# Kernel optimization log

Hardware: AMD Instinct MI355X
Metric: run time of the kernel (lower is better)

The kernel has to match this reference:

```python
import jax, jax.numpy as jnp
import numpy as np

B, T, HM = 2, 2048, 1024
HEADS = 16
DK = (HM // 2) // HEADS   # expand_k = 0.5 -> key_dim 512, per-head 32
DV = HM // HEADS          # expand_v = 1.0 -> per-head 64
LOW_RANK = 16             # gate low-rank dim (fla default)
GATE_NORM = 16.0          # gate_logit_normalizer (fla default)
EPS = 1e-5


def setup_inputs() -> dict:
    key = jax.random.key(0)
    ks = jax.random.split(key, 12)
    def p(k, shape, s=0.02):
        return jax.random.normal(k, shape, jnp.float32) * s
    return dict(
        x=jax.random.normal(ks[0], (B, T, HM), jnp.float32),
        ln_w=jnp.ones((HM,), jnp.float32), ln_b=jnp.zeros((HM,), jnp.float32),
        Wq=p(ks[1], (HM, HEADS * DK)), Wk=p(ks[2], (HM, HEADS * DK)),
        Wv=p(ks[3], (HM, HEADS * DV)),
        gk_w1=p(ks[4], (HM, LOW_RANK)), gk_w2=p(ks[5], (LOW_RANK, HEADS * DK)),
        gk_b2=jnp.zeros((HEADS * DK,), jnp.float32),
        Wg=p(ks[6], (HM, HEADS * DV)), rms_w=jnp.ones((DV,), jnp.float32),
        Wo=p(ks[7], (HEADS * DV, HM)),
        W1=p(ks[8], (HM, 2 * HM)), b1=jnp.zeros((2 * HM,), jnp.float32),
        W2=p(ks[9], (2 * HM, HM)), b2=jnp.zeros((HM,), jnp.float32),
    )


def _ln(x, w, b):
    m = x.mean(-1, keepdims=True)
    v = ((x - m) ** 2).mean(-1, keepdims=True)
    return (x - m) * jax.lax.rsqrt(v + EPS) * w + b


def _rms(x, w):
    return x * jax.lax.rsqrt((x * x).mean(-1, keepdims=True) + EPS) * w


def _gla(q, k, v, gk):
    # gated linear attention recurrence:
    # S_t = diag(exp(gk_t)) S_{t-1} + k_t v_t^T ;  o_t = q_t S_t
    # q,k,gk: [B,T,H,DK], v: [B,T,H,DV]
    def step(S, inp):
        qt, kt, vt, gt = inp
        S = jnp.exp(gt)[..., None] * S + kt[..., None] * vt[..., None, :]
        return S, jnp.einsum('bhk,bhkv->bhv', qt, S)
    xs = tuple(jnp.moveaxis(a, 1, 0) for a in (q, k, v, gk))
    S0 = jnp.zeros((q.shape[0], q.shape[2], q.shape[3], v.shape[3]), q.dtype)
    _, o = jax.lax.scan(step, S0, xs)
    return jnp.moveaxis(o, 0, 1)


def reference(x, ln_w, ln_b, Wq, Wk, Wv, gk_w1, gk_w2, gk_b2, Wg, rms_w, Wo, W1, b1, W2, b2):
    Bb, Tt, _ = x.shape
    h = _ln(x, ln_w, ln_b)
    q = (h @ Wq).reshape(Bb, Tt, HEADS, DK)
    k = (h @ Wk).reshape(Bb, Tt, HEADS, DK)
    v = (h @ Wv).reshape(Bb, Tt, HEADS, DV)
    gk = (jax.nn.log_sigmoid((h @ gk_w1) @ gk_w2 + gk_b2) / GATE_NORM)
    gk = gk.reshape(Bb, Tt, HEADS, DK)
    o = _gla(q * (DK ** -0.5), k, v, gk)
    # output gate: RMSNorm(o) * swish(g)  (FusedRMSNormSwishGate)
    g = (h @ Wg).reshape(Bb, Tt, HEADS, DV)
    o = _rms(o, rms_w) * (g * jax.nn.sigmoid(g))
    x = x + o.reshape(Bb, Tt, HEADS * DV) @ Wo
    h2 = _ln(x, ln_w, ln_b)  # same shared norm module
    return x + jax.nn.gelu(h2 @ W1 + b1, approximate=False) @ W2 + b2
```

## Files before the change

### kernel.cpp

```cpp
#include <hip/hip_runtime.h>
#include <hip/hip_bf16.h>
#include <math.h>


using bf16 = __hip_bfloat16;
typedef __attribute__((ext_vector_type(8))) short bf16x8;
typedef __attribute__((ext_vector_type(4))) float f32x4;

#define BT 4096
#define HM 1024
#define DK 32
#define DV 64
#define NC 32
#define CHK 64

#if defined(__has_builtin)
#if __has_builtin(__builtin_amdgcn_global_load_lds)
#define HAVE_GLDS 1
#endif
#endif

#ifdef HAVE_GLDS
#define GLDS16(g, l) __builtin_amdgcn_global_load_lds( \
    (const __attribute__((address_space(1))) unsigned int*)(g), \
    (__attribute__((address_space(3))) unsigned int*)(l), 16, 0, 0)
#else
#define GLDS16(g, l) (*(int4*)(l) = *(const int4*)(g))
#endif

__device__ __forceinline__ float b2f(bf16 v) { return __bfloat162float(v); }
__device__ __forceinline__ bf16 f2b(float v) { return __float2bfloat16(v); }
__device__ __forceinline__ float clampf(float v, float lim) {
    return fminf(fmaxf(v, -lim), lim);
}
__device__ __forceinline__ float lo16(unsigned int u) {
    union { unsigned int i; float f; } c; c.i = u << 16; return c.f;
}
__device__ __forceinline__ float hi16(unsigned int u) {
    union { unsigned int i; float f; } c; c.i = u & 0xffff0000u; return c.f;
}
__device__ __forceinline__ void acc8(float a, uint4 r, float* o) {
    o[0] += a * lo16(r.x); o[1] += a * hi16(r.x);
    o[2] += a * lo16(r.y); o[3] += a * hi16(r.y);
    o[4] += a * lo16(r.z); o[5] += a * hi16(r.z);
    o[6] += a * lo16(r.w); o[7] += a * hi16(r.w);
}

__global__ __launch_bounds__(256) void detect_dtype(
    const unsigned int* __restrict__ x, int* __restrict__ flag)
{
    int tid = threadIdx.x;
    int cnt = 0;
    for (int i = 0; i < 16; ++i) {
        unsigned int w = x[tid * 16 + i];
        unsigned int e_lo = (w >> 7) & 0xffu;
        unsigned int e_hi = (w >> 23) & 0xffu;
        cnt += (e_lo >= 110 && e_lo <= 135 && e_hi >= 110 && e_hi <= 135) ? 1 : 0;
    }
    __shared__ int red[256];
    red[tid] = cnt;
    __syncthreads();
    for (int s = 128; s > 0; s >>= 1) {
        if (tid < s) red[tid] += red[tid + s];
        __syncthreads();
    }
    if (tid == 0) *flag = (red[0] > 2048) ? 1 : 0;
}

struct SmallCvt { const void* s[8]; bf16* d[8]; int n[8]; };
__global__ __launch_bounds__(256) void cvt_small(SmallCvt sc, const int* __restrict__ flag)
{
    bool isb = (*flag != 0);
    int stride = gridDim.x * 256;
    #pragma unroll
    for (int seg = 0; seg < 8; ++seg) {
        int n = sc.n[seg];
        for (int i = blockIdx.x * 256 + threadIdx.x; i < n; i += stride) {
            if (isb) ((ushort*)sc.d[seg])[i] = ((const ushort*)sc.s[seg])[i];
            else     sc.d[seg][i] = f2b(((const float*)sc.s[seg])[i]);
        }
    }
}

struct TDesc { const void* src; ushort* dst; int R, C, tile0; };
struct TAll { TDesc d[7]; };
__global__ __launch_bounds__(256) void transpose_all(
    TAll ta, const int* __restrict__ flag)
{
    bool isb = (*flag != 0);
    int bid = blockIdx.x;
    int seg = 0;
    #pragma unroll
    for (int i = 1; i < 7; ++i) if (bid >= ta.d[i].tile0) seg = i;
    const void* src = ta.d[seg].src;
    ushort* dst = ta.d[seg].dst;
    int R = ta.d[seg].R, C = ta.d[seg].C;
    int t = bid - ta.d[seg].tile0;
    int tilesX = C >> 5;
    int c0 = (t % tilesX) * 32, r0 = (t / tilesX) * 32;

    __shared__ ushort tile[32][33];
    int x = threadIdx.x, y = threadIdx.y;
    #pragma unroll
    for (int dy = 0; dy < 32; dy += 8) {
        size_t idx = (size_t)(r0 + y + dy) * C + c0 + x;
        ushort v;
        if (isb) v = ((const ushort*)src)[idx];
        else { bf16 tb = f2b(((const float*)src)[idx]); v = *(ushort*)&tb; }
        tile[y + dy][x] = v;
    }
    __syncthreads();
    #pragma unroll
    for (int dy = 0; dy < 32; dy += 8)
        dst[(size_t)(c0 + y + dy) * R + r0 + x] = tile[x][y + dy];
}

template <int DO_GK>
__global__ __launch_bounds__(256) void ln_kernel(
    const void* __restrict__ x, const bf16* __restrict__ w, const bf16* __restrict__ b,
    bf16* __restrict__ out, const int* __restrict__ flag, int force,
    const bf16* __restrict__ w1, const bf16* __restrict__ w2,
    const bf16* __restrict__ b2i, bf16* __restrict__ gkout)
{
    bool isb = (force >= 0) ? (force != 0) : (*flag != 0);
    size_t base = (size_t)blockIdx.x * HM;
    int tid = threadIdx.x;
    float v[4], s = 0.f, s2 = 0.f;
    #pragma unroll
    for (int u = 0; u < 4; ++u) {
        size_t idx = base + tid + u * 256;
        float f = isb ? b2f(((const bf16*)x)[idx]) : ((const float*)x)[idx];
        v[u] = f; s += f; s2 += f * f;
    }
    #pragma unroll
    for (int off = 32; off >= 1; off >>= 1) {
        s  += __shfl_down(s, off);
        s2 += __shfl_down(s2, off);
    }
    __shared__ float ra[4], rb[4];
    __shared__ float hrow[1024];
    int wave = tid >> 6;
    if ((tid & 63) == 0) { ra[wave] = s; rb[wave] = s2; }
    __syncthreads();
    s = ra[0] + ra[1] + ra[2] + ra[3];
    s2 = rb[0] + rb[1] + rb[2] + rb[3];
    float mean = s * (1.f / HM);
    float var = fmaxf(s2 * (1.f / HM) - mean * mean, 0.f);
    float rs = rsqrtf(var + 1e-5f);
    #pragma unroll
    for (int u = 0; u < 4; ++u) {
        int col = tid + u * 256;
        float h = (v[u] - mean) * rs * b2f(w[col]) + b2f(b[col]);
        out[base + col] = f2b(h);
        if constexpr (DO_GK) hrow[col] = h;
    }
    if constexpr (DO_GK) {
        __syncthreads();
        int d = tid & 15, seg = tid >> 4;
        float sg = 0.f;
        #pragma unroll 8
        for (int j = 0; j < 64; ++j) {
            int i = seg * 64 + j;
            sg += hrow[i] * b2f(w1[i * 16 + d]);
        }
        __shared__ float red[256];
        __shared__ float g1[16];
        red[tid] = sg;
        __syncthreads();
        if (tid < 16) {
            float t = 0.f;
            #pragma unroll
            for (int s2i = 0; s2i < 16; ++s2i) t += red[s2i * 16 + tid];
            g1[tid] = t;
        }
        __syncthreads();
        #pragma unroll
        for (int rep = 0; rep < 2; ++rep) {
            int n = tid + rep * 256;
            float z = b2f(b2i[n]);
            #pragma unroll
            for (int r = 0; r < 16; ++r) z += g1[r] * b2f(w2[r * 512 + n]);
            z = clampf(z, 30.f);
            float ls = (z >= 0.f) ? -log1pf(expf(-z)) : (z - log1pf(expf(z)));
            gkout[blockIdx.x * 512 + n] = f2b(ls * 0.0625f);
        }
    }
}

template <int BN, int MODE>
__global__ __launch_bounds__(512, 2) void gemm8p(
    const bf16* __restrict__ A, const bf16* __restrict__ Wt,
    const bf16* __restrict__ bias, const void* __restrict__ resid,
    void* __restrict__ out, int M, int N, int K, const int* __restrict__ oflag)
{
    constexpr int NFRAG  = BN / 128;
    constexpr int BLOADS = (BN == 256) ? 2 : 1;

    extern __shared__ ushort sm[];
    ushort* smA = sm;
    ushort* smB = sm + 32768;

    int tid = threadIdx.x;
    int wid = tid >> 6, l = tid & 63;
    int wm = wid >> 2, wn = wid & 3;
    int r16 = l & 15, quad = l >> 4;
    int bm = blockIdx.x * 256, bn = blockIdx.y * BN;
    bool isb = false;
    if constexpr (MODE == 1 || MODE == 3) isb = (*oflag != 0);

    const ushort* Au = (const ushort*)A;
    const ushort* Wu = (const ushort*)Wt;
    const int NT = K >> 6;

    auto stageA = [&](int t, int h) {
        #pragma unroll
        for (int i = 0; i < 2; ++i) {
            int j = i * 512 + tid;
            int lr = j >> 3, slot = j & 7;
            int r = (lr & 63) + h * 64 + (lr >> 6) * 128;
            int sl = slot ^ (r & 7);
            const ushort* g = Au + (size_t)(bm + r) * K + t * 64 + sl * 8;
            GLDS16(g, &smA[(t & 1) * 16384 + r * 64 + slot * 8]);
        }
    };
    auto stageB = [&](int t, int h) {
        #pragma unroll
        for (int i = 0; i < BLOADS; ++i) {
            int j = i * 512 + tid;
            int lr = j >> 3, slot = j & 7;
            int r = (BN == 256) ? ((lr & 31) + h * 32 + (lr >> 5) * 64)
                                : ((lr & 15) + h * 16 + (lr >> 4) * 32);
            int sl = slot ^ (r & 7);
            const ushort* g = Wu + (size_t)(bn + r) * K + t * 64 + sl * 8;
            GLDS16(g, &smB[(t & 1) * (BN * 64) + r * 64 + slot * 8]);
        }
    };

    int colx0 = (quad * 8) ^ ((r16 & 7) * 8);
    int colx1 = colx0 ^ 32;

    f32x4 acc[8][BN / 64] = {};

    stageA(0, 0); stageB(0, 0); stageA(0, 1); stageB(0, 1);
    if (NT > 1) { stageA(1, 0); stageB(1, 1); }
    if constexpr (BN == 256) asm volatile("s_waitcnt vmcnt(4)" ::: "memory");
    else                     asm volatile("s_waitcnt vmcnt(3)" ::: "memory");
    __builtin_amdgcn_s_barrier();

    for (int t = 0; t < NT; ++t) {
        const int abase = (t & 1) * 16384;
        const int bbase = (t & 1) * (BN * 64);
        #pragma unroll
        for (int q = 0; q < 4; ++q) {
            const int mh = q >> 1;
            const int nh = (q == 1 || q == 2) ? 1 : 0;
            bf16x8 af[2][4], bw[2][NFRAG];
            #pragma unroll
            for (int mf = 0; mf < 4; ++mf) {
                int r = wm * 128 + mh * 64 + mf * 16 + r16;
                af[0][mf] = *(const bf16x8*)&smA[abase + r * 64 + colx0];
                af[1][mf] = *(const bf16x8*)&smA[abase + r * 64 + colx1];
            }
            #pragma unroll
            for (int nf = 0; nf < NFRAG; ++nf) {
                int r = wn * (BN / 4) + nh * (NFRAG * 16) + nf * 16 + r16;
                bw[0][nf] = *(const bf16x8*)&smB[bbase + r * 64 + colx0];
                bw[1][nf] = *(const bf16x8*)&smB[bbase + r * 64 + colx1];
            }
            if (q == 0) { if (t + 1 < NT) stageA(t + 1, 1); }
            if (q == 1) { if (t + 1 < NT) stageB(t + 1, 0); }
            if (q == 2) { if (t + 2 < NT) stageA(t + 2, 0); }
            if (q == 3) { if (t + 2 < NT) stageB(t + 2, 1); }
            __builtin_amdgcn_s_barrier();
            asm volatile("s_waitcnt lgkmcnt(0)" ::: "memory");
            __builtin_amdgcn_s_setprio(1);
            #pragma unroll
            for (int mf = 0; mf < 4; ++mf)
                #pragma unroll
                for (int nf = 0; nf < NFRAG; ++nf) {
                    f32x4& a = acc[mh * 4 + mf][nh * NFRAG + nf];
                    a = __builtin_amdgcn_mfma_f32_16x16x32_bf16(af[0][mf], bw[0][nf], a, 0, 0, 0);
                    a = __builtin_amdgcn_mfma_f32_16x16x32_bf16(af[1][mf], bw[1][nf], a, 0, 0, 0);
                }
            __builtin_amdgcn_s_setprio(0);
            if (q == 3) {
                if (t + 2 < NT) {
                    if constexpr (BN == 256) asm volatile("s_waitcnt vmcnt(4)" ::: "memory");
                    else                     asm volatile("s_waitcnt vmcnt(3)" ::: "memory");
                } else {
                    asm volatile("s_waitcnt vmcnt(0)" ::: "memory");
                }
            }
            __builtin_amdgcn_s_barrier();
        }
    }

    #pragma unroll
    for (int am = 0; am < 8; ++am) {
        int row0 = bm + wm * 128 + am * 16 + quad * 4;
        #pragma unroll
        for (int an = 0; an < BN / 64; ++an) {
            int col = bn + wn * (BN / 4) + an * 16 + r16;
            #pragma unroll
            for (int r = 0; r < 4; ++r) {
                size_t idx = (size_t)(row0 + r) * N + col;
                float v = acc[am][an][r];
                if constexpr (MODE == 0) {
                    ((bf16*)out)[idx] = f2b(clampf(v, 1e4f));
                } else if constexpr (MODE == 2) {
                    float t = clampf(v + b2f(bias[col]), 50.f);
                    ((bf16*)out)[idx] = f2b(0.5f * t * (1.f + erff(t * 0.70710678f)));
                } else if constexpr (MODE == 1) {
                    float rv = isb ? b2f(((const bf16*)resid)[idx])
                                   : ((const float*)resid)[idx];
                    ((float*)out)[idx] = clampf(rv + v, 1e5f);
                } else {
                    float t = clampf(v + b2f(bias[col]) + ((const float*)resid)[idx], 2e5f);
                    if (isb) ((bf16*)out)[idx] = f2b(t);
                    else     ((float*)out)[idx] = t;
                }
            }
        }
    }
}

__global__ __launch_bounds__(256) void gla_phase1(
    const bf16* __restrict__ gkb, const bf16* __restrict__ qvg,
    float* __restrict__ clbuf, float* __restrict__ Dbuf, float* __restrict__ Pbuf)
{
    int bh = blockIdx.x, c = blockIdx.y;
    int b = bh >> 4, hh = bh & 15;
    int row0 = b * 2048 + c * CHK;
    __shared__ float glog[CHK][DK + 1];
    __shared__ float wk[CHK][DK + 1];
    __shared__ float segsum[8][DK + 1];
    __shared__ __align__(16) ushort vt[CHK][DV];
    int tid = threadIdx.x;
    int k = tid & 31, i8 = (tid >> 5) * 8;
    int seg = tid >> 5;
    #pragma unroll
    for (int u = 0; u < 8; ++u) {
        int i = i8 + u;
        float g = b2f(gkb[(size_t)(row0 + i) * 512 + hh * 32 + k]);
        glog[i][k] = fminf(fmaxf(g, -2.f), 0.f);
    }
    {
        int cc = tid & 7, ii = tid >> 3;
        #pragma unroll
        for (int h = 0; h < 2; ++h) {
            int i = ii + h * 32;
            uint4 val = *(const uint4*)((const ushort*)qvg + (size_t)(row0 + i) * 3072 + 1024 + hh * 64 + cc * 8);
            *(uint4*)&vt[i][cc * 8] = val;
        }
    }
    __syncthreads();
    {
        float run = 0.f;
        #pragma unroll
        for (int u = 0; u < 8; ++u) {
            run += glog[i8 + u][k];
            glog[i8 + u][k] = run;
        }
        segsum[seg][k] = run;
    }
    __syncthreads();
    {
        float off = 0.f;
        for (int s = 0; s < seg; ++s) off += segsum[s][k];
        #pragma unroll
        for (int u = 0; u < 8; ++u) glog[i8 + u][k] += off;
    }
    __syncthreads();
    #pragma unroll
    for (int u = 0; u < 8; ++u) {
        int i = i8 + u;
        float cl = glog[i][k];
        float cl63 = glog[CHK - 1][k];
        clbuf[(size_t)(row0 + i) * 512 + hh * 32 + k] = cl;
        wk[i][k] = expf(fmaxf(cl63 - cl, -60.f)) *
            b2f(qvg[(size_t)(row0 + i) * 3072 + 512 + hh * 32 + k]);
    }
    if (tid < 32) Dbuf[(size_t)(bh * 32 + c) * 32 + tid] = expf(glog[CHK - 1][tid]);
    __syncthreads();
    int kk = tid >> 3, v8 = (tid & 7) * 8;
    float acc[8] = {};
    for (int j = 0; j < CHK; ++j) {
        float w = wk[j][kk];
        uint4 raw = *(const uint4*)&vt[j][v8];
        acc8(w, raw, acc);
    }
    float* Pp = Pbuf + (size_t)(bh * 32 + c) * 2048 + kk * 64 + v8;
    #pragma unroll
    for (int u = 0; u < 8; ++u) Pp[u] = acc[u];
}

__global__ __launch_bounds__(256) void gla_scan(
    const float* __restrict__ Pbuf, const float* __restrict__ Dbuf,
    float* __restrict__ Sbuf)
{
    int bh = blockIdx.x >> 3, vg8 = blockIdx.x & 7;
    int kk = threadIdx.x >> 3, vv = vg8 * 8 + (threadIdx.x & 7);
    float S = 0.f;
    for (int c = 0; c < NC; ++c) {
        size_t idx = (size_t)(bh * 32 + c) * 2048 + kk * 64 + vv;
        float P = Pbuf[idx];
        float D = Dbuf[(size_t)(bh * 32 + c) * 32 + kk];
        Sbuf[idx] = S;
        S = D * S + P;
    }
}

__global__ __launch_bounds__(256) void gla_phase3(
    const bf16* __restrict__ qvg,
    const float* __restrict__ clbuf, const float* __restrict__ Sbuf,
    const bf16* __restrict__ rmsw, bf16* __restrict__ obuf)
{
    int bh = blockIdx.x, c = blockIdx.y;
    int b = bh >> 4, hh = bh & 15;
    int row0 = b * 2048 + c * CHK;
    __shared__ float qs[CHK][36], ks[CHK][36];
    __shared__ float S0[DK][68];
    __shared__ float Amat[CHK][CHK + 1];
    __shared__ __align__(16) ushort vt[CHK][DV];
    int tid = threadIdx.x;
    {
        int k = tid & 31, i8 = (tid >> 5) * 8;
        #pragma unroll
        for (int u = 0; u < 8; ++u) {
            int i = i8 + u;
            size_t r = (size_t)(row0 + i);
            int col = hh * 32 + k;
            float cl = fmaxf(clbuf[r * 512 + col], -60.f);
            qs[i][k] = b2f(qvg[r * 3072 + col]) * expf(cl) * 0.17677669529663687f;
            ks[i][k] = b2f(qvg[r * 3072 + 512 + col]) * expf(-cl);
        }
    }
    {
        int cc = tid & 7, ii = tid >> 3;
        #pragma unroll
        for (int h = 0; h < 2; ++h) {
            int i = ii + h * 32;
            uint4 val = *(const uint4*)((const ushort*)qvg + (size_t)(row0 + i) * 3072 + 1024 + hh * 64 + cc * 8);
            *(uint4*)&vt[i][cc * 8] = val;
        }
    }
    {
        int kk = tid >> 3, v8 = (tid & 7) * 8;
        const float* Sp = Sbuf + (size_t)(bh * 32 + c) * 2048 + kk * 64 + v8;
        *(f32x4*)&S0[kk][v8]     = *(const f32x4*)Sp;
        *(f32x4*)&S0[kk][v8 + 4] = *(const f32x4*)(Sp + 4);
    }
    __syncthreads();
    int i = tid >> 2, jb = tid & 3;
    for (int jj = 0; jj < 16; ++jj) {
        int j = jb + jj * 4;
        float d = 0.f;
        if (j <= i) {
            const f32x4* qp = (const f32x4*)qs[i];
            const f32x4* kp = (const f32x4*)ks[j];
            #pragma unroll
            for (int q8 = 0; q8 < 8; ++q8) {
                f32x4 a = qp[q8], bq = kp[q8];
                d += a.x * bq.x + a.y * bq.y + a.z * bq.z + a.w * bq.w;
            }
        }
        Amat[i][j] = d;
    }
    __syncthreads();
    float o[16] = {};
    int vv = jb * 16;
    for (int j = 0; j < CHK; ++j) {
        float a = Amat[i][j];
        uint4 r0 = *(const uint4*)&vt[j][vv];
        uint4 r1 = *(const uint4*)&vt[j][vv + 8];
        acc8(a, r0, o);
        acc8(a, r1, o + 8);
    }
    #pragma unroll
    for (int kk = 0; kk < DK; ++kk) {
        float qv = qs[i][kk];
        const f32x4* Sp = (const f32x4*)&S0[kk][vv];
        #pragma unroll
        for (int q4 = 0; q4 < 4; ++q4) {
            f32x4 sv = Sp[q4];
            o[q4 * 4 + 0] += qv * sv.x; o[q4 * 4 + 1] += qv * sv.y;
            o[q4 * 4 + 2] += qv * sv.z; o[q4 * 4 + 3] += qv * sv.w;
        }
    }
    float ss = 0.f;
    #pragma unroll
    for (int u = 0; u < 16; ++u) ss += o[u] * o[u];
    ss += __shfl_xor(ss, 1);
    ss += __shfl_xor(ss, 2);
    float sc = rsqrtf(fmaxf(ss, 0.f) * (1.f / DV) + 1e-5f);
    size_t r = (size_t)(row0 + i);
    #pragma unroll
    for (int u = 0; u < 16; ++u) {
        float g = b2f(qvg[r * 3072 + 2048 + hh * 64 + vv + u]);
        float sw = g / (1.f + expf(-g));
        obuf[r * 1024 + hh * 64 + vv + u] = f2b(clampf(o[u] * sc * b2f(rmsw[vv + u]) * sw, 3e4f));
    }
}

extern "C" void kernel_launch(void* const* d_in, const int* in_sizes, int n_in,
                              void* d_out, int out_size, void* d_ws, size_t ws_size,
                              hipStream_t stream) {
    (void)in_sizes; (void)n_in; (void)out_size; (void)ws_size;

    char* ws = (char*)d_ws;
    const size_t MB = 1024 * 1024;
    const size_t KB = 1024;
    bf16*  WqkT = (bf16*)(ws + 0);
    bf16*  WkT  = (bf16*)(ws + 1 * MB);
    bf16*  WvgT = (bf16*)(ws + 2 * MB);
    bf16*  WgT  = (bf16*)(ws + 4 * MB);
    bf16*  WoT  = (bf16*)(ws + 6 * MB);
    bf16*  W1T  = (bf16*)(ws + 8 * MB);
    bf16*  W2T  = (bf16*)(ws + 12 * MB);
    bf16*  hbuf = (bf16*)(ws + 16 * MB);
    bf16*  qvg  = (bf16*)(ws + 24 * MB);
    bf16*  gkb  = (bf16*)(ws + 48 * MB);
    float* clbf = (float*)(ws + 52 * MB);
    float* Dbuf = (float*)(ws + 60 * MB);
    float* Pbuf = (float*)(ws + 61 * MB);
    float* Sbuf = (float*)(ws + 69 * MB);
    bf16*  obuf = (bf16*)(ws + 61 * MB);
    float* ybuf = (float*)(ws + 32 * MB);
    bf16*  f1   = (bf16*)(ws + 48 * MB);
    bf16*  clnw = (bf16*)(ws + 85 * MB);
    bf16*  clnb = (bf16*)(ws + 85 * MB + 64 * KB);
    bf16*  cgw1 = (bf16*)(ws + 85 * MB + 128 * KB);
    bf16*  cgw2 = (bf16*)(ws + 85 * MB + 192 * KB);
    bf16*  cgb2 = (bf16*)(ws + 85 * MB + 256 * KB);
    bf16*  crms = (bf16*)(ws + 85 * MB + 320 * KB);
    bf16*  cb1  = (bf16*)(ws + 85 * MB + 384 * KB);
    bf16*  cb2  = (bf16*)(ws + 85 * MB + 448 * KB);
    int*   flag = (int*)(ws + 85 * MB + 512 * KB);

    hipLaunchKernelGGL(detect_dtype, dim3(1), dim3(256), 0, stream,
                       (const unsigned int*)d_in[0], flag);

    SmallCvt sc;
    sc.s[0] = d_in[1];  sc.d[0] = clnw; sc.n[0] = 1024;
    sc.s[1] = d_in[2];  sc.d[1] = clnb; sc.n[1] = 1024;
    sc.s[2] = d_in[6];  sc.d[2] = cgw1; sc.n[2] = 16384;
    sc.s[3] = d_in[7];  sc.d[3] = cgw2; sc.n[3] = 8192;
    sc.s[4] = d_in[8];  sc.d[4] = cgb2; sc.n[4] = 512;
    sc.s[5] = d_in[10]; sc.d[5] = crms; sc.n[5] = 64;
    sc.s[6] = d_in[13]; sc.d[6] = cb1;  sc.n[6] = 2048;
    sc.s[7] = d_in[15]; sc.d[7] = cb2;  sc.n[7] = 1024;
    hipLaunchKernelGGL(cvt_small, dim3(64), dim3(256), 0, stream, sc, flag);

    TAll ta;
    ta.d[0] = { d_in[3],  (ushort*)WqkT, 1024, 512,  0 };
    ta.d[1] = { d_in[4],  (ushort*)WkT,  1024, 512,  512 };
    ta.d[2] = { d_in[5],  (ushort*)WvgT, 1024, 1024, 1024 };
    ta.d[3] = { d_in[9],  (ushort*)WgT,  1024, 1024, 2048 };
    ta.d[4] = { d_in[11], (ushort*)WoT,  1024, 1024, 3072 };
    ta.d[5] = { d_in[12], (ushort*)W1T,  1024, 2048, 4096 };
    ta.d[6] = { d_in[14], (ushort*)W2T,  2048, 1024, 6144 };
    hipLaunchKernelGGL(transpose_all, dim3(8192), dim3(32, 8), 0, stream, ta, flag);

    hipLaunchKernelGGL((ln_kernel<1>), dim3(BT), dim3(256), 0, stream,
                       d_in[0], clnw, clnb, hbuf, (const int*)flag, -1,
                       cgw1, cgw2, cgb2, gkb);

    hipLaunchKernelGGL((gemm8p<256, 0>), dim3(16, 12), dim3(512), 131072, stream,
                       hbuf, WqkT, (const bf16*)nullptr, nullptr, (void*)qvg,
                       BT, 3072, 1024, flag);

    hipLaunchKernelGGL(gla_phase1, dim3(32, 32), dim3(256), 0, stream, gkb, qvg, clbf, Dbuf, Pbuf);
    hipLaunchKernelGGL(gla_scan, dim3(256), dim3(256), 0, stream, Pbuf, Dbuf, Sbuf);
    hipLaunchKernelGGL(gla_phase3, dim3(32, 32), dim3(256), 0, stream, qvg, clbf, Sbuf, crms, obuf);

    hipLaunchKernelGGL((gemm8p<128, 1>), dim3(16, 8), dim3(512), 98304, stream,
                       obuf, WoT, (const bf16*)nullptr, (const void*)d_in[0], (void*)ybuf,
                       BT, 1024, 1024, flag);
    hipLaunchKernelGGL((ln_kernel<0>), dim3(BT), dim3(256), 0, stream,
                       (const void*)ybuf, clnw, clnb, hbuf, (const int*)flag, 0,
                       (const bf16*)nullptr, (const bf16*)nullptr, (const bf16*)nullptr, (bf16*)nullptr);
    hipLaunchKernelGGL((gemm8p<128, 2>), dim3(16, 16), dim3(512), 98304, stream,
                       hbuf, W1T, cb1, nullptr, (void*)f1, BT, 2048, 1024, flag);
    hipLaunchKernelGGL((gemm8p<128, 3>), dim3(16, 8), dim3(512), 98304, stream,
                       f1, W2T, cb2, (const void*)ybuf, d_out, BT, 1024, 2048, flag);
}
```

Before: 396.6 us.

## Restructure GEMM inner loop into K-halves with reused B fragments and static LDS

The GEMM main loop now splits each 64-wide K tile into two 32-wide halves across the four sub-steps. All N fragments of B are loaded once per half and reused across both M halves, instead of loading A and B for both K halves at every sub-step. The staging order of A and B loads and the vmcnt waits are reordered to match, and shared memory moves from dynamic to static arrays. This lowers LDS read traffic per MFMA but holds more B registers live, which may affect occupancy or stall behaviour.

After: 397.8 us. No clear change (+0.3%).

```diff
diff --git a/kernel.cpp b/kernel.cpp
--- a/kernel.cpp
+++ b/kernel.cpp
@@ -193,12 +193,11 @@
     const bf16* __restrict__ bias, const void* __restrict__ resid,
     void* __restrict__ out, int M, int N, int K, const int* __restrict__ oflag)
 {
-    constexpr int NFRAG  = BN / 128;
-    constexpr int BLOADS = (BN == 256) ? 2 : 1;
-
-    extern __shared__ ushort sm[];
-    ushort* smA = sm;
-    ushort* smB = sm + 32768;
+    constexpr int NF = BN / 64;
+    constexpr int BLOADS = BN / 128;
+
+    __shared__ __align__(16) ushort smA[2 * 256 * 64];
+    __shared__ __align__(16) ushort smB[2 * BN * 64];
 
     int tid = threadIdx.x;
     int wid = tid >> 6, l = tid & 63;
@@ -236,40 +235,41 @@
         }
     };
 
-    int colx0 = (quad * 8) ^ ((r16 & 7) * 8);
-    int colx1 = colx0 ^ 32;
-
-    f32x4 acc[8][BN / 64] = {};
-
-    stageA(0, 0); stageB(0, 0); stageA(0, 1); stageB(0, 1);
-    if (NT > 1) { stageA(1, 0); stageB(1, 1); }
+    const int colx0 = (quad ^ (r16 & 7)) * 8;
+
+    f32x4 acc[8][NF] = {};
+
+    stageA(0, 0); stageA(0, 1); stageB(0, 0); stageB(0, 1);
+    if (NT > 1) { stageB(1, 0); stageB(1, 1); }
     if constexpr (BN == 256) asm volatile("s_waitcnt vmcnt(4)" ::: "memory");
-    else                     asm volatile("s_waitcnt vmcnt(3)" ::: "memory");
+    else                     asm volatile("s_waitcnt vmcnt(2)" ::: "memory");
     __builtin_amdgcn_s_barrier();
 
     for (int t = 0; t < NT; ++t) {
         const int abase = (t & 1) * 16384;
         const int bbase = (t & 1) * (BN * 64);
+        bf16x8 bw[2][NF];
         #pragma unroll
         for (int q = 0; q < 4; ++q) {
             const int mh = q >> 1;
-            const int nh = (q == 1 || q == 2) ? 1 : 0;
-            bf16x8 af[2][4], bw[2][NFRAG];
+            const int kh = q & 1;
+            const int colx = kh ? (colx0 ^ 32) : colx0;
+            bf16x8 af[4];
             #pragma unroll
             for (int mf = 0; mf < 4; ++mf) {
                 int r = wm * 128 + mh * 64 + mf * 16 + r16;
-                af[0][mf] = *(const bf16x8*)&smA[abase + r * 64 + colx0];
-                af[1][mf] = *(const bf16x8*)&smA[abase + r * 64 + colx1];
+                af[mf] = *(const bf16x8*)&smA[abase + r * 64 + colx];
             }
-            #pragma unroll
-            for (int nf = 0; nf < NFRAG; ++nf) {
-                int r = wn * (BN / 4) + nh * (NFRAG * 16) + nf * 16 + r16;
-                bw[0][nf] = *(const bf16x8*)&smB[bbase + r * 64 + colx0];
-                bw[1][nf] = *(const bf16x8*)&smB[bbase + r * 64 + colx1];
+            if (q < 2) {
+                #pragma unroll
+                for (int nf = 0; nf < NF; ++nf) {
+                    int r = wn * (BN / 4) + nf * 16 + r16;
+                    bw[kh][nf] = *(const bf16x8*)&smB[bbase + r * 64 + colx];
+                }
             }
-            if (q == 0) { if (t + 1 < NT) stageA(t + 1, 1); }
-            if (q == 1) { if (t + 1 < NT) stageB(t + 1, 0); }
-            if (q == 2) { if (t + 2 < NT) stageA(t + 2, 0); }
+            if (q == 0) { if (t + 1 < NT) stageA(t + 1, 0); }
+            if (q == 1) { if (t + 1 < NT) stageA(t + 1, 1); }
+            if (q == 2) { if (t + 2 < NT) stageB(t + 2, 0); }
             if (q == 3) { if (t + 2 < NT) stageB(t + 2, 1); }
             __builtin_amdgcn_s_barrier();
             asm volatile("s_waitcnt lgkmcnt(0)" ::: "memory");
@@ -277,16 +277,14 @@
             #pragma unroll
             for (int mf = 0; mf < 4; ++mf)
                 #pragma unroll
-                for (int nf = 0; nf < NFRAG; ++nf) {
-                    f32x4& a = acc[mh * 4 + mf][nh * NFRAG + nf];
-                    a = __builtin_amdgcn_mfma_f32_16x16x32_bf16(af[0][mf], bw[0][nf], a, 0, 0, 0);
-                    a = __builtin_amdgcn_mfma_f32_16x16x32_bf16(af[1][mf], bw[1][nf], a, 0, 0, 0);
-                }
+                for (int nf = 0; nf < NF; ++nf)
+                    acc[mh * 4 + mf][nf] = __builtin_amdgcn_mfma_f32_16x16x32_bf16(
+                        af[mf], bw[kh][nf], acc[mh * 4 + mf][nf], 0, 0, 0);
             __builtin_amdgcn_s_setprio(0);
             if (q == 3) {
                 if (t + 2 < NT) {
                     if constexpr (BN == 256) asm volatile("s_waitcnt vmcnt(4)" ::: "memory");
-                    else                     asm volatile("s_waitcnt vmcnt(3)" ::: "memory");
+                    else                     asm volatile("s_waitcnt vmcnt(2)" ::: "memory");
                 } else {
                     asm volatile("s_waitcnt vmcnt(0)" ::: "memory");
                 }
@@ -299,7 +297,7 @@
     for (int am = 0; am < 8; ++am) {
         int row0 = bm + wm * 128 + am * 16 + quad * 4;
         #pragma unroll
-        for (int an = 0; an < BN / 64; ++an) {
+        for (int an = 0; an < NF; ++an) {
             int col = bn + wn * (BN / 4) + an * 16 + r16;
             #pragma unroll
             for (int r = 0; r < 4; ++r) {
@@ -565,7 +563,7 @@
                        d_in[0], clnw, clnb, hbuf, (const int*)flag, -1,
                        cgw1, cgw2, cgb2, gkb);
 
-    hipLaunchKernelGGL((gemm8p<256, 0>), dim3(16, 12), dim3(512), 131072, stream,
+    hipLaunchKernelGGL((gemm8p<256, 0>), dim3(16, 12), dim3(512), 0, stream,
                        hbuf, WqkT, (const bf16*)nullptr, nullptr, (void*)qvg,
                        BT, 3072, 1024, flag);
 
@@ -573,14 +571,14 @@
     hipLaunchKernelGGL(gla_scan, dim3(256), dim3(256), 0, stream, Pbuf, Dbuf, Sbuf);
     hipLaunchKernelGGL(gla_phase3, dim3(32, 32), dim3(256), 0, stream, qvg, clbf, Sbuf, crms, obuf);
 
-    hipLaunchKernelGGL((gemm8p<128, 1>), dim3(16, 8), dim3(512), 98304, stream,
+    hipLaunchKernelGGL((gemm8p<128, 1>), dim3(16, 8), dim3(512), 0, stream,
                        obuf, WoT, (const bf16*)nullptr, (const void*)d_in[0], (void*)ybuf,
                        BT, 1024, 1024, flag);
     hipLaunchKernelGGL((ln_kernel<0>), dim3(BT), dim3(256), 0, stream,
                        (const void*)ybuf, clnw, clnb, hbuf, (const int*)flag, 0,
                        (const bf16*)nullptr, (const bf16*)nullptr, (const bf16*)nullptr, (bf16*)nullptr);
-    hipLaunchKernelGGL((gemm8p<128, 2>), dim3(16, 16), dim3(512), 98304, stream,
+    hipLaunchKernelGGL((gemm8p<128, 2>), dim3(16, 16), dim3(512), 0, stream,
                        hbuf, W1T, cb1, nullptr, (void*)f1, BT, 2048, 1024, flag);
-    hipLaunchKernelGGL((gemm8p<128, 3>), dim3(16, 8), dim3(512), 98304, stream,
+    hipLaunchKernelGGL((gemm8p<128, 3>), dim3(16, 8), dim3(512), 0, stream,
                        f1, W2T, cb2, (const void*)ybuf, d_out, BT, 1024, 2048, flag);
 }
```

## Replace QKV/G projection GEMM with simpler 128x128-tile kernel for more blocks

Applied to the files above, without the earlier changes.

Adds a new 256-thread GEMM kernel with 128x128 tiles and static 32KB LDS, loading A and B via global_load_lds and using 16x16x32 bf16 MFMA. It replaces the 256-wide 512-thread gemm8p for the fused Q/K/V/G projection, raising the grid from 192 to 768 blocks to better fill the CUs. The new kernel has no double buffering (sync before and after each K step), which may expose load latency. It also drops the oflag parameter the old kernel took.

New measurement: 461.7 us. 16.4% more time.

```diff
diff --git a/kernel.cpp b/kernel.cpp
--- a/kernel.cpp
+++ b/kernel.cpp
@@ -183,6 +183,77 @@
             z = clampf(z, 30.f);
             float ls = (z >= 0.f) ? -log1pf(expf(-z)) : (z - log1pf(expf(z)));
             gkout[blockIdx.x * 512 + n] = f2b(ls * 0.0625f);
+        }
+    }
+}
+
+template <int MODE>
+__global__ __launch_bounds__(256) void gemm128(
+    const bf16* __restrict__ A, const bf16* __restrict__ Wt,
+    const bf16* __restrict__ bias, void* __restrict__ out, int M, int N, int K)
+{
+    __shared__ __align__(16) ushort As[128 * 64];
+    __shared__ __align__(16) ushort Bs[128 * 64];
+    int tid = threadIdx.x;
+    int w = tid >> 6, l = tid & 63;
+    int bm = blockIdx.x * 128, bn = blockIdx.y * 128;
+    int row16 = l & 15, quad = l >> 4;
+
+    const ushort* Au = (const ushort*)A;
+    const ushort* Wu = (const ushort*)Wt;
+
+    int ab = (w >> 1) * 4;
+    int bb = (w & 1) * 4;
+
+    f32x4 acc[4][4] = {};
+    for (int k0 = 0; k0 < K; k0 += 64) {
+        #pragma unroll
+        for (int p = 0; p < 2; ++p) {
+            #pragma unroll
+            for (int i = 0; i < 2; ++i) {
+                int j = i * 4 + w;
+                const ushort* gA = Au + (size_t)(bm + j * 16 + row16) * K
+                                   + k0 + p * 32 + quad * 8;
+                GLDS16(gA, &As[p * 4096 + j * 512 + l * 8]);
+                const ushort* gB = Wu + (size_t)(bn + j * 16 + row16) * K
+                                   + k0 + p * 32 + quad * 8;
+                GLDS16(gB, &Bs[p * 4096 + j * 512 + l * 8]);
+            }
+        }
+        __syncthreads();
+        #pragma unroll
+        for (int p = 0; p < 2; ++p) {
+            int fo = p * 4096 + quad * 128 + row16 * 8;
+            bf16x8 af[4], bw[4];
+            #pragma unroll
+            for (int mi = 0; mi < 4; ++mi) af[mi] = *(const bf16x8*)&As[(ab + mi) * 512 + fo];
+            #pragma unroll
+            for (int ni = 0; ni < 4; ++ni) bw[ni] = *(const bf16x8*)&Bs[(bb + ni) * 512 + fo];
+            #pragma unroll
+            for (int mi = 0; mi < 4; ++mi)
+                #pragma unroll
+                for (int ni = 0; ni < 4; ++ni)
+                    acc[mi][ni] = __builtin_amdgcn_mfma_f32_16x16x32_bf16(af[mi], bw[ni], acc[mi][ni], 0, 0, 0);
+        }
+        __syncthreads();
+    }
+    #pragma unroll
+    for (int mi = 0; mi < 4; ++mi) {
+        #pragma unroll
+        for (int ni = 0; ni < 4; ++ni) {
+            int col = bn + (w & 1) * 64 + ni * 16 + row16;
+            #pragma unroll
+            for (int r = 0; r < 4; ++r) {
+                int row = bm + (w >> 1) * 64 + mi * 16 + quad * 4 + r;
+                size_t idx = (size_t)row * N + col;
+                float v = acc[mi][ni][r];
+                if constexpr (MODE == 0) {
+                    ((bf16*)out)[idx] = f2b(clampf(v, 1e4f));
+                } else {
+                    float t = clampf(v + b2f(bias[col]), 50.f);
+                    ((bf16*)out)[idx] = f2b(0.5f * t * (1.f + erff(t * 0.70710678f)));
+                }
+            }
         }
     }
 }
@@ -565,9 +636,8 @@
                        d_in[0], clnw, clnb, hbuf, (const int*)flag, -1,
                        cgw1, cgw2, cgb2, gkb);
 
-    hipLaunchKernelGGL((gemm8p<256, 0>), dim3(16, 12), dim3(512), 131072, stream,
-                       hbuf, WqkT, (const bf16*)nullptr, nullptr, (void*)qvg,
-                       BT, 3072, 1024, flag);
+    hipLaunchKernelGGL((gemm128<0>), dim3(32, 24), dim3(256), 0, stream,
+                       hbuf, WqkT, (const bf16*)nullptr, (void*)qvg, BT, 3072, 1024);
 
     hipLaunchKernelGGL(gla_phase1, dim3(32, 32), dim3(256), 0, stream, gkb, qvg, clbf, Dbuf, Pbuf);
     hipLaunchKernelGGL(gla_scan, dim3(256), dim3(256), 0, stream, Pbuf, Dbuf, Sbuf);
```
